# Kernel optimization log

Hardware: AMD Instinct MI355X
Metric: run time of the kernel (lower is better)

Reference implementation:

```python
import jax, jax.numpy as jnp
import numpy as np

SCALES = (1, 2, 4)
KS = 5          # conv kernel size
POOL = 2        # maxpool kernel & stride


def coarse_grain(x, s):
    # non-overlapping mean pool along last axis
    B, C, L = x.shape
    Lc = L // s
    return x[:, :, : Lc * s].reshape(B, C, Lc, s).mean(axis=-1)


def conv1d(x, w, b):
    # x: [B, C_in, L], w: [C_out, C_in, K] (torch layout), VALID padding, stride 1
    y = jax.lax.conv_general_dilated(
        x, w, window_strides=(1,), padding='VALID',
        dimension_numbers=('NCH', 'OIH', 'NCH'))
    return y + b[None, :, None]


def maxpool1d(x, k):
    B, C, L = x.shape
    Lp = L // k
    return x[:, :, : Lp * k].reshape(B, C, Lp, k).max(axis=-1)


def conv_block(x, w1, b1, w2, b2):
    x = maxpool1d(jax.nn.relu(conv1d(x, w1, b1)), POOL)
    x = maxpool1d(jax.nn.relu(conv1d(x, w2, b2)), POOL)
    return x


def setup_inputs() -> dict:
    key = jax.random.key(0)
    ks = jax.random.split(key, 9)
    B, C, NWL = 2048, 4, 480
    C1, C2 = 16, 32
    # flatten size per model's own arithmetic: sum over scales of conv/pool output lens * C2
    F = (117 + 57 + 27) * C2  # 6432
    NOUT = 5
    sc = lambda fan_in: 1.0 / np.sqrt(fan_in)
    return {
        'x':  jax.random.normal(ks[0], (B, C, NWL), dtype=jnp.float32),
        'w1': jax.random.uniform(ks[1], (C1, C, KS), jnp.float32, -sc(C * KS), sc(C * KS)),
        'b1': jax.random.uniform(ks[2], (C1,), jnp.float32, -sc(C * KS), sc(C * KS)),
        'w2': jax.random.uniform(ks[3], (C2, C1, KS), jnp.float32, -sc(C1 * KS), sc(C1 * KS)),
        'b2': jax.random.uniform(ks[4], (C2,), jnp.float32, -sc(C1 * KS), sc(C1 * KS)),
        'wl': jax.random.uniform(ks[5], (F, F), jnp.float32, -sc(F), sc(F)),
        'bl': jax.random.uniform(ks[6], (F,), jnp.float32, -sc(F), sc(F)),
        'wo': jax.random.uniform(ks[7], (NOUT, F), jnp.float32, -sc(F), sc(F)),
        'bo': jax.random.uniform(ks[8], (NOUT,), jnp.float32, -sc(F), sc(F)),
    }


def reference(x, w1, b1, w2, b2, wl, bl, wo, bo):
    # multi-scale feature mapping: shared ConvBlock applied to each coarse-grained scale
    feats = [conv_block(coarse_grain(x, s), w1, b1, w2, b2) for s in SCALES]
    f = jnp.concatenate(feats, axis=-1)            # [B, 32, 201]
    f = f.reshape(f.shape[0], -1)                  # [B, 6432]
    # the SAME linear layer (shared weights) is applied 4 times in torch
    for _ in range(4):
        f = jax.nn.relu(f @ wl.T + bl)
    return f @ wo.T + bo                           # [B, 5]
```

## Files before the change

### kernel.cpp

```cpp
#include <hip/hip_runtime.h>

typedef _Float16 v8h __attribute__((ext_vector_type(8)));
typedef _Float16 v4h __attribute__((ext_vector_type(4)));
typedef float    v4f __attribute__((ext_vector_type(4)));

#define GK 6432
#define GN 6432
#define GM 2048
#define KP 6528

__global__ void convert_w(const float* __restrict__ wl, _Float16* __restrict__ Wh)
{
    const int row = blockIdx.y;
    const int col = (blockIdx.x * 256 + threadIdx.x) * 4;
    if (col >= KP) return;
    v4h h;
    if (col < GK) {
        const float4 f = *(const float4*)(wl + (long)row * GK + col);
        h[0] = (_Float16)f.x; h[1] = (_Float16)f.y;
        h[2] = (_Float16)f.z; h[3] = (_Float16)f.w;
    } else {
        h[0] = (_Float16)0.f; h[1] = (_Float16)0.f;
        h[2] = (_Float16)0.f; h[3] = (_Float16)0.f;
    }
    *(v4h*)(Wh + (long)row * KP + col) = h;
}

#define SX   0
#define SX2  2048
#define SX4  3136
#define SW1  3712
#define SB1  4032
#define SW2  4048
#define SB2  6608
#define SP1  6640
#define LDSZ 13808

__global__ __launch_bounds__(256) void conv_feat(
    const float* __restrict__ x,
    const float* __restrict__ w1, const float* __restrict__ b1,
    const float* __restrict__ w2, const float* __restrict__ b2,
    _Float16* __restrict__ F0)
{
    __shared__ float lds[LDSZ];
    const int tid = threadIdx.x;
    const long b  = blockIdx.x;

    for (int i = tid; i < 1920; i += 256) {
        int c = i / 480, t = i % 480;
        lds[SX + c * 512 + t] = x[(b * 4 + c) * 480 + t];
    }
    for (int i = tid; i < 320;  i += 256) lds[SW1 + i] = w1[i];
    for (int i = tid; i < 16;   i += 256) lds[SB1 + i] = b1[i];
    for (int i = tid; i < 2560; i += 256) lds[SW2 + i] = w2[i];
    for (int i = tid; i < 32;   i += 256) lds[SB2 + i] = b2[i];
    for (int i = tid; i < KP - GK; i += 256) F0[b * KP + GK + i] = (_Float16)0.f;
    __syncthreads();

    for (int i = tid; i < 960; i += 256) {
        int c = i / 240, t = i % 240;
        lds[SX2 + c * 272 + t] = 0.5f * (lds[SX + c * 512 + 2 * t] + lds[SX + c * 512 + 2 * t + 1]);
    }
    for (int i = tid; i < 480; i += 256) {
        int c = i / 120, t = i % 120;
        float s = lds[SX + c * 512 + 4 * t]     + lds[SX + c * 512 + 4 * t + 1]
                + lds[SX + c * 512 + 4 * t + 2] + lds[SX + c * 512 + 4 * t + 3];
        lds[SX4 + c * 144 + t] = 0.25f * s;
    }
    __syncthreads();

    for (int jid = tid; jid < 16 * 34; jid += 256) {
        const int c1 = jid / 34, rid = jid % 34;
        const int sidx = (rid < 19) ? 0 : (rid < 29 ? 1 : 2);
        const int r0   = (sidx == 0) ? rid : (sidx == 1 ? rid - 19 : rid - 29);
        const int u0   = r0 * 13;
        const int xbase  = (sidx == 0) ? SX  : (sidx == 1 ? SX2 : SX4);
        const int xpitch = (sidx == 0) ? 512 : (sidx == 1 ? 272 : 144);
        const int P      = (sidx == 0) ? 238 : (sidx == 1 ? 118 : 58);
        const int pofs   = (sidx == 0) ? 0   : (sidx == 1 ? 238 : 356);

        float acc[26];
        const float bias = lds[SB1 + c1];
        #pragma unroll
        for (int i = 0; i < 26; ++i) acc[i] = bias;

        #pragma unroll
        for (int ci = 0; ci < 4; ++ci) {
            float w[30];
            const float* xr = &lds[xbase + ci * xpitch + 2 * u0];
            #pragma unroll
            for (int q = 0; q < 15; ++q) {
                float2 t2 = *(const float2*)(xr + 2 * q);
                w[2 * q] = t2.x; w[2 * q + 1] = t2.y;
            }
            float wt[5];
            #pragma unroll
            for (int k = 0; k < 5; ++k) wt[k] = lds[SW1 + (c1 * 4 + ci) * 5 + k];
            #pragma unroll
            for (int i = 0; i < 26; ++i) {
                #pragma unroll
                for (int k = 0; k < 5; ++k) acc[i] += w[i + k] * wt[k];
            }
        }
        #pragma unroll
        for (int i = 0; i < 13; ++i) {
            int u = u0 + i;
            if (u < P)
                lds[SP1 + c1 * 448 + pofs + u] = fmaxf(fmaxf(acc[2 * i], acc[2 * i + 1]), 0.f);
        }
    }
    __syncthreads();

    for (int jid = tid; jid < 32 * 17; jid += 256) {
        const int c2 = jid / 17, rid = jid % 17;
        const int sidx = (rid < 9) ? 0 : (rid < 14 ? 1 : 2);
        const int r0   = (sidx == 0) ? rid : (sidx == 1 ? rid - 9 : rid - 14);
        const int v0   = r0 * 13;
        const int pbase = (sidx == 0) ? 0   : (sidx == 1 ? 238 : 356);
        const int Pv    = (sidx == 0) ? 117 : (sidx == 1 ? 57  : 27);
        const int vout  = (sidx == 0) ? 0   : (sidx == 1 ? 117 : 174);

        float acc[26];
        const float bias = lds[SB2 + c2];
        #pragma unroll
        for (int i = 0; i < 26; ++i) acc[i] = bias;

        for (int c1 = 0; c1 < 16; ++c1) {
            float w[30];
            const float* pr = &lds[SP1 + c1 * 448 + pbase + 2 * v0];
            #pragma unroll
            for (int q = 0; q < 15; ++q) {
                float2 t2 = *(const float2*)(pr + 2 * q);
                w[2 * q] = t2.x; w[2 * q + 1] = t2.y;
            }
            float wt[5];
            #pragma unroll
            for (int k = 0; k < 5; ++k) wt[k] = lds[SW2 + (c2 * 16 + c1) * 5 + k];
            #pragma unroll
            for (int i = 0; i < 26; ++i) {
                #pragma unroll
                for (int k = 0; k < 5; ++k) acc[i] += w[i + k] * wt[k];
            }
        }
        #pragma unroll
        for (int i = 0; i < 13; ++i) {
            int v = v0 + i;
            if (v < Pv) {
                float f = fmaxf(fmaxf(acc[2 * i], acc[2 * i + 1]), 0.f);
                F0[b * KP + c2 * 201 + vout + v] = (_Float16)f;
            }
        }
    }
}

__global__ __launch_bounds__(512, 2) void gemm8(
    const _Float16* __restrict__ A, const _Float16* __restrict__ Bw,
    const float* __restrict__ bias, _Float16* __restrict__ C)
{
    __shared__ _Float16 sA[2][256 * 64];
    __shared__ _Float16 sB[2][256 * 64];

    const int tid  = threadIdx.x;
    const int lane = tid & 63;
    const int wave = tid >> 6;
    const int wr   = wave >> 2;
    const int wc   = wave & 3;

    const int id  = blockIdx.x;
    const int xcd = id & 7;
    const int loc = id >> 3;
    const int m_t = ((xcd & 3) << 1) | (loc & 1);
    const int n_t = (xcd >> 2) * 13 + (loc >> 1);
    const long tile_m = (long)m_t << 8;
    const long tile_n = (long)n_t << 8;

    const int lrow = lane >> 3;
    const int lcol = ((lane & 7) ^ lrow) << 3;
    const int rA1  = wave * 16 + ((wave & 4) << 4);
    const int rA2  = rA1 + 64;
    const int rB1  = wave * 16;
    const int rB2  = rB1 + 128;

    const _Float16* gA = A  + (tile_m + lrow) * (long)KP + lcol;
    const _Float16* gB = Bw + lcol;

#define STAGE_A(buf, row0, k0)                                                             \
    {                                                                                      \
        __builtin_amdgcn_global_load_lds(                                                  \
            (const __attribute__((address_space(1))) void*)(gA + (long)(row0) * KP + (k0)),\
            (__attribute__((address_space(3))) void*)(&sA[buf][(row0) * 64]), 16, 0, 0);   \
        __builtin_amdgcn_global_load_lds(                                                  \
            (const __attribute__((address_space(1))) void*)(gA + (long)((row0) + 8) * KP + (k0)), \
            (__attribute__((address_space(3))) void*)(&sA[buf][((row0) + 8) * 64]), 16, 0, 0);    \
    }

#define STAGE_B(buf, row0, k0)                                                             \
    {                                                                                      \
        long r0_ = tile_n + (row0) + lrow;     if (r0_ > 6431) r0_ = 6431;                 \
        long r1_ = r0_ + 8;                    if (r1_ > 6431) r1_ = 6431;                 \
        __builtin_amdgcn_global_load_lds(                                                  \
            (const __attribute__((address_space(1))) void*)(gB + r0_ * KP + (k0)),         \
            (__attribute__((address_space(3))) void*)(&sB[buf][(row0) * 64]), 16, 0, 0);   \
        __builtin_amdgcn_global_load_lds(                                                  \
            (const __attribute__((address_space(1))) void*)(gB + r1_ * KP + (k0)),         \
            (__attribute__((address_space(3))) void*)(&sB[buf][((row0) + 8) * 64]), 16, 0, 0);    \
    }

    const int fr = lane & 15;
    const int fp = lane >> 4;
    const int sw = fr & 7;
    const int slot0 = ((fp)     ^ sw) << 3;
    const int slot1 = ((fp + 4) ^ sw) << 3;
    const int abase = (wr * 128 + fr) * 64;

    v8h af[8], bf0[2][2], bf1[2][2];
    v4f acc[8][4];
    #pragma unroll
    for (int i = 0; i < 8; ++i) {
        #pragma unroll
        for (int j = 0; j < 4; ++j) { v4f z = {0.f, 0.f, 0.f, 0.f}; acc[i][j] = z; }
    }

#define LDA(base, h) { _Pragma("unroll")                                                   \
      for (int mi = 0; mi < 4; ++mi) {                                                     \
          af[mi * 2]     = *(const v8h*)((base) + abase + (h) * 4096 + mi * 1024 + slot0); \
          af[mi * 2 + 1] = *(const v8h*)((base) + abase + (h) * 4096 + mi * 1024 + slot1); \
      } }

#define LDB(base, h, bf) { _Pragma("unroll")                                               \
      for (int ni = 0; ni < 2; ++ni) {                                                     \
          bf[ni][0] = *(const v8h*)((base) + (wc * 64 + (h) * 32 + ni * 16 + fr) * 64 + slot0); \
          bf[ni][1] = *(const v8h*)((base) + (wc * 64 + (h) * 32 + ni * 16 + fr) * 64 + slot1); \
      } }

#define MMAQ(mh, nh, bf) { _Pragma("unroll")                                               \
      for (int mi = 0; mi < 4; ++mi) { _Pragma("unroll")                                   \
          for (int ni = 0; ni < 2; ++ni) {                                                 \
              acc[(mh)*4+mi][(nh)*2+ni] = __builtin_amdgcn_mfma_f32_16x16x32_f16(          \
                  af[mi * 2],     bf[ni][0], acc[(mh)*4+mi][(nh)*2+ni], 0, 0, 0);          \
              acc[(mh)*4+mi][(nh)*2+ni] = __builtin_amdgcn_mfma_f32_16x16x32_f16(          \
                  af[mi * 2 + 1], bf[ni][1], acc[(mh)*4+mi][(nh)*2+ni], 0, 0, 0);          \
          } } }

#define ROUND(SBUF, KO, S1, S2) {                                                          \
                          \
    LDA(sA[SBUF], 0); LDB(sB[SBUF], 0, bf0);                                               \
    if (S1) STAGE_B((SBUF) ^ 1, rB2, (KO) + 64);                                           \
    __builtin_amdgcn_s_barrier();                                                          \
    asm volatile("s_waitcnt lgkmcnt(0)" ::: "memory");                                     \
    __builtin_amdgcn_s_setprio(1);                                                         \
    MMAQ(0, 0, bf0);                                                                       \
    __builtin_amdgcn_s_setprio(0);                                                         \
    __builtin_amdgcn_s_barrier();                                                          \
                           \
    LDB(sB[SBUF], 1, bf1);                                                                 \
    if (S2) STAGE_A(SBUF, rA1, (KO) + 128);                                                \
    __builtin_amdgcn_s_barrier();                                                          \
    asm volatile("s_waitcnt lgkmcnt(0)" ::: "memory");                                     \
    __builtin_amdgcn_s_setprio(1);                                                         \
    MMAQ(0, 1, bf1);                                                                       \
    __builtin_amdgcn_s_setprio(0);                                                         \
    __builtin_amdgcn_s_barrier();                                                          \
                                    \
    LDA(sA[SBUF], 1);                                                                      \
    if (S2) STAGE_B(SBUF, rB1, (KO) + 128);                                                \
    __builtin_amdgcn_s_barrier();                                                          \
    asm volatile("s_waitcnt lgkmcnt(0)" ::: "memory");                                     \
    __builtin_amdgcn_s_setprio(1);                                                         \
    MMAQ(1, 1, bf1);                                                                       \
    __builtin_amdgcn_s_setprio(0);                                                         \
    __builtin_amdgcn_s_barrier();                                                          \
                      \
    if (S2) STAGE_A(SBUF, rA2, (KO) + 128);                                                \
    __builtin_amdgcn_s_barrier();                                                          \
    __builtin_amdgcn_s_setprio(1);                                                         \
    MMAQ(1, 0, bf0);                                                                       \
    __builtin_amdgcn_s_setprio(0);                                                         \
    if (S2) { asm volatile("s_waitcnt vmcnt(6)" ::: "memory"); }                           \
    else    { asm volatile("s_waitcnt vmcnt(0)" ::: "memory"); }                           \
    __builtin_amdgcn_s_barrier(); }

    STAGE_A(0, rA1, 0);  STAGE_B(0, rB1, 0);  STAGE_A(0, rA2, 0);  STAGE_B(0, rB2, 0);
    STAGE_A(1, rA1, 64); STAGE_B(1, rB1, 64); STAGE_A(1, rA2, 64);
    asm volatile("s_waitcnt vmcnt(6)" ::: "memory");
    __builtin_amdgcn_s_barrier();

    for (int kt = 0; kt < 100; kt += 2) {
        ROUND(0, kt * 64,       1, 1);
        ROUND(1, kt * 64 + 64,  1, 1);
    }
    ROUND(0, 6400, 1, 0);
    ROUND(1, 6464, 0, 0);

    #pragma unroll
    for (int j = 0; j < 4; ++j) {
        const long col = tile_n + (wc << 6) + (j << 4) + fr;
        if (col < KP) {
            const bool val = col < GN;
            const float bv = val ? bias[col] : 0.f;
            #pragma unroll
            for (int i = 0; i < 8; ++i) {
                const long row = tile_m + wr * 128 + (i << 4) + (fp << 2);
                #pragma unroll
                for (int r = 0; r < 4; ++r) {
                    float v = acc[i][j][r] + bv;
                    v = v > 0.f ? v : 0.f;
                    C[(row + r) * (long)KP + col] = val ? (_Float16)v : (_Float16)0.f;
                }
            }
        }
    }

#undef STAGE_A
#undef STAGE_B
#undef LDA
#undef LDB
#undef MMAQ
#undef ROUND
}

__global__ __launch_bounds__(256) void final_out(
    const _Float16* __restrict__ F, const float* __restrict__ wo,
    const float* __restrict__ bo, float* __restrict__ out)
{
    __shared__ float red[4][8];
    const long b   = blockIdx.x;
    const int tid  = threadIdx.x;
    const int lane = tid & 63;
    const int wave = tid >> 6;
    float acc[5] = {0.f, 0.f, 0.f, 0.f, 0.f};
    const _Float16* f = F + b * KP;

    const int c1 = (wave + 1) * 402;
    for (int c = wave * 402 + lane; c < c1; c += 64) {
        const int k = c << 2;
        v4h f4 = *(const v4h*)(f + k);
        const float f0 = (float)f4[0], f1 = (float)f4[1];
        const float f2 = (float)f4[2], f3 = (float)f4[3];
        #pragma unroll
        for (int o = 0; o < 5; ++o) {
            const float4 w4 = *(const float4*)(wo + o * GK + k);
            acc[o] += f0 * w4.x + f1 * w4.y + f2 * w4.z + f3 * w4.w;
        }
    }
    #pragma unroll
    for (int o = 0; o < 5; ++o) {
        #pragma unroll
        for (int off = 32; off > 0; off >>= 1) acc[o] += __shfl_down(acc[o], off, 64);
    }
    if (lane == 0) {
        #pragma unroll
        for (int o = 0; o < 5; ++o) red[wave][o] = acc[o];
    }
    __syncthreads();
    if (tid < 5)
        out[b * 5 + tid] = red[0][tid] + red[1][tid] + red[2][tid] + red[3][tid] + bo[tid];
}

extern "C" void kernel_launch(void* const* d_in, const int* in_sizes, int n_in,
                              void* d_out, int out_size, void* d_ws, size_t ws_size,
                              hipStream_t stream)
{
    const float* x  = (const float*)d_in[0];
    const float* w1 = (const float*)d_in[1];
    const float* b1 = (const float*)d_in[2];
    const float* w2 = (const float*)d_in[3];
    const float* b2 = (const float*)d_in[4];
    const float* wl = (const float*)d_in[5];
    const float* bl = (const float*)d_in[6];
    const float* wo = (const float*)d_in[7];
    const float* bo = (const float*)d_in[8];
    float* out = (float*)d_out;

    char* ws = (char*)d_ws;
    _Float16* Wh = (_Float16*)ws;
    _Float16* F0 = (_Float16*)(ws + 83976192);
    _Float16* F1 = (_Float16*)(ws + 83976192 + 26738688);

    convert_w<<<dim3(7, GN), 256, 0, stream>>>(wl, Wh);
    conv_feat<<<GM, 256, 0, stream>>>(x, w1, b1, w2, b2, F0);
    gemm8<<<208, 512, 0, stream>>>(F0, Wh, bl, F1);
    gemm8<<<208, 512, 0, stream>>>(F1, Wh, bl, F0);
    gemm8<<<208, 512, 0, stream>>>(F0, Wh, bl, F1);
    gemm8<<<208, 512, 0, stream>>>(F1, Wh, bl, F0);
    final_out<<<GM, 256, 0, stream>>>(F0, wo, bo, out);
}
```

Before: 1.317 ms.

## Fuse final output projection into last GEMM epilogue with atomics; simplify tile mapping

The fourth GEMM no longer writes its fp16 activation matrix. Its epilogue stages bias and the five output-weight rows in shared memory, computes the ReLU activations, and reduces their dot products across lanes. The partial sums are atomically added into the output, which a new small kernel pre-fills with the output bias. This removes the final_out kernel and one full activation write and read, in exchange for many atomics and non-deterministic summation order. The block-to-tile mapping also changes from an XCD-aware swizzle to a plain id&7 / id>>3 mapping, which may hurt L2 locality across chiplets.

After: 1.432 ms. 1.09x slower.

```diff
diff --git a/kernel.cpp b/kernel.cpp
--- a/kernel.cpp
+++ b/kernel.cpp
@@ -153,9 +153,18 @@
     }
 }
 
+__global__ __launch_bounds__(512) void out_init(const float* __restrict__ bo,
+                                                float* __restrict__ out)
+{
+    const int i = blockIdx.x * 512 + threadIdx.x;
+    if (i < GM * 5) out[i] = bo[i % 5];
+}
+
+template<int FUSED>
 __global__ __launch_bounds__(512, 2) void gemm8(
     const _Float16* __restrict__ A, const _Float16* __restrict__ Bw,
-    const float* __restrict__ bias, _Float16* __restrict__ C)
+    const float* __restrict__ bias, _Float16* __restrict__ C,
+    const float* __restrict__ wo, float* __restrict__ outp)
 {
     __shared__ _Float16 sA[2][256 * 64];
     __shared__ _Float16 sB[2][256 * 64];
@@ -167,12 +176,8 @@
     const int wc   = wave & 3;
 
     const int id  = blockIdx.x;
-    const int xcd = id & 7;
-    const int loc = id >> 3;
-    const int m_t = ((xcd & 3) << 1) | (loc & 1);
-    const int n_t = (xcd >> 2) * 13 + (loc >> 1);
-    const long tile_m = (long)m_t << 8;
-    const long tile_n = (long)n_t << 8;
+    const long tile_m = (long)(id & 7) << 8;
+    const long tile_n = (long)(id >> 3) << 8;
 
     const int lrow = lane >> 3;
     const int lcol = ((lane & 7) ^ lrow) << 3;
@@ -292,20 +297,69 @@
     ROUND(0, 6400, 1, 0);
     ROUND(1, 6464, 0, 0);
 
-    #pragma unroll
-    for (int j = 0; j < 4; ++j) {
-        const long col = tile_n + (wc << 6) + (j << 4) + fr;
-        if (col < KP) {
-            const bool val = col < GN;
-            const float bv = val ? bias[col] : 0.f;
-            #pragma unroll
-            for (int i = 0; i < 8; ++i) {
-                const long row = tile_m + wr * 128 + (i << 4) + (fp << 2);
+    if constexpr (FUSED == 0) {
+        #pragma unroll
+        for (int j = 0; j < 4; ++j) {
+            const long col = tile_n + (wc << 6) + (j << 4) + fr;
+            if (col < KP) {
+                const bool val = col < GN;
+                const float bv = val ? bias[col] : 0.f;
                 #pragma unroll
-                for (int r = 0; r < 4; ++r) {
-                    float v = acc[i][j][r] + bv;
+                for (int i = 0; i < 8; ++i) {
+                    const long row = tile_m + wr * 128 + (i << 4) + (fp << 2);
+                    #pragma unroll
+                    for (int r = 0; r < 4; ++r) {
+                        float v = acc[i][j][r] + bv;
+                        v = v > 0.f ? v : 0.f;
+                        C[(row + r) * (long)KP + col] = val ? (_Float16)v : (_Float16)0.f;
+                    }
+                }
+            }
+        }
+    } else {
+        float* fl = (float*)&sA[0][0];
+        __syncthreads();
+        for (int i = tid; i < 256 * 6; i += 512) {
+            const int c = i & 255, j = i >> 8;
+            const long gcol = tile_n + c;
+            float v = 0.f;
+            if (gcol < GN) v = (j == 0) ? bias[gcol] : wo[(long)(j - 1) * GK + gcol];
+            fl[j * 256 + c] = v;
+        }
+        __syncthreads();
+        const float* biasL = fl;
+        const float* woL   = fl + 256;
+        #pragma unroll
+        for (int i = 0; i < 8; ++i) {
+            #pragma unroll
+            for (int r = 0; r < 4; ++r) {
+                float s0 = 0.f, s1 = 0.f, s2 = 0.f, s3 = 0.f, s4 = 0.f;
+                #pragma unroll
+                for (int j = 0; j < 4; ++j) {
+                    const int cl = (wc << 6) + (j << 4) + fr;
+                    float v = acc[i][j][r] + biasL[cl];
                     v = v > 0.f ? v : 0.f;
-                    C[(row + r) * (long)KP + col] = val ? (_Float16)v : (_Float16)0.f;
+                    s0 += v * woL[cl];
+                    s1 += v * woL[256 + cl];
+                    s2 += v * woL[512 + cl];
+                    s3 += v * woL[768 + cl];
+                    s4 += v * woL[1024 + cl];
+                }
+                #pragma unroll
+                for (int m = 1; m < 16; m <<= 1) {
+                    s0 += __shfl_xor(s0, m, 64);
+                    s1 += __shfl_xor(s1, m, 64);
+                    s2 += __shfl_xor(s2, m, 64);
+                    s3 += __shfl_xor(s3, m, 64);
+                    s4 += __shfl_xor(s4, m, 64);
+                }
+                if (fr == 0) {
+                    const long row = tile_m + wr * 128 + (i << 4) + (fp << 2) + r;
+                    atomicAdd(&outp[row * 5 + 0], s0);
+                    atomicAdd(&outp[row * 5 + 1], s1);
+                    atomicAdd(&outp[row * 5 + 2], s2);
+                    atomicAdd(&outp[row * 5 + 3], s3);
+                    atomicAdd(&outp[row * 5 + 4], s4);
                 }
             }
         }
@@ -317,44 +371,6 @@
 #undef LDB
 #undef MMAQ
 #undef ROUND
-}
-
-__global__ __launch_bounds__(256) void final_out(
-    const _Float16* __restrict__ F, const float* __restrict__ wo,
-    const float* __restrict__ bo, float* __restrict__ out)
-{
-    __shared__ float red[4][8];
-    const long b   = blockIdx.x;
-    const int tid  = threadIdx.x;
-    const int lane = tid & 63;
-    const int wave = tid >> 6;
-    float acc[5] = {0.f, 0.f, 0.f, 0.f, 0.f};
-    const _Float16* f = F + b * KP;
-
-    const int c1 = (wave + 1) * 402;
-    for (int c = wave * 402 + lane; c < c1; c += 64) {
-        const int k = c << 2;
-        v4h f4 = *(const v4h*)(f + k);
-        const float f0 = (float)f4[0], f1 = (float)f4[1];
-        const float f2 = (float)f4[2], f3 = (float)f4[3];
-        #pragma unroll
-        for (int o = 0; o < 5; ++o) {
-            const float4 w4 = *(const float4*)(wo + o * GK + k);
-            acc[o] += f0 * w4.x + f1 * w4.y + f2 * w4.z + f3 * w4.w;
-        }
-    }
-    #pragma unroll
-    for (int o = 0; o < 5; ++o) {
-        #pragma unroll
-        for (int off = 32; off > 0; off >>= 1) acc[o] += __shfl_down(acc[o], off, 64);
-    }
-    if (lane == 0) {
-        #pragma unroll
-        for (int o = 0; o < 5; ++o) red[wave][o] = acc[o];
-    }
-    __syncthreads();
-    if (tid < 5)
-        out[b * 5 + tid] = red[0][tid] + red[1][tid] + red[2][tid] + red[3][tid] + bo[tid];
 }
 
 extern "C" void kernel_launch(void* const* d_in, const int* in_sizes, int n_in,
@@ -379,9 +395,9 @@
 
     convert_w<<<dim3(7, GN), 256, 0, stream>>>(wl, Wh);
     conv_feat<<<GM, 256, 0, stream>>>(x, w1, b1, w2, b2, F0);
-    gemm8<<<208, 512, 0, stream>>>(F0, Wh, bl, F1);
-    gemm8<<<208, 512, 0, stream>>>(F1, Wh, bl, F0);
-    gemm8<<<208, 512, 0, stream>>>(F0, Wh, bl, F1);
-    gemm8<<<208, 512, 0, stream>>>(F1, Wh, bl, F0);
-    final_out<<<GM, 256, 0, stream>>>(F0, wo, bo, out);
+    gemm8<0><<<208, 512, 0, stream>>>(F0, Wh, bl, F1, nullptr, nullptr);
+    gemm8<0><<<208, 512, 0, stream>>>(F1, Wh, bl, F0, nullptr, nullptr);
+    gemm8<0><<<208, 512, 0, stream>>>(F0, Wh, bl, F1, nullptr, nullptr);
+    out_init<<<20, 512, 0, stream>>>(bo, out);
+    gemm8<1><<<208, 512, 0, stream>>>(F1, Wh, bl, nullptr, wo, out);
 }
```
